# Optimization experiments

Measured on AMD Instinct MI355X. Metric: run time of the kernel, lower is better.

The kernel has to match this reference:

```python
import jax, jax.numpy as jnp
import numpy as np

EPS = 1e-5          # InstanceNorm eps (torch default)
KERNEL = 25         # moving_avg_kernel_size
TAU = 1.0           # gumbel softmax temperature
REGIME_NUM = 8


def _inorm(x):
    # InstanceNorm1d without affine on (N, C, L): normalize over last dim (biased var)
    m = x.mean(-1, keepdims=True)
    v = ((x - m) ** 2).mean(-1, keepdims=True)
    return (x - m) * jax.lax.rsqrt(v + EPS)


def _lbr(x, W, b):
    # Linear -> InstanceNorm (over last dim) -> exact GELU
    return jax.nn.gelu(_inorm(x @ W + b), approximate=False)


def _moving_avg(x, k):
    # x: (B, L, C); edge-replicate pad (k-1)//2 on both sides, sliding mean via cumsum
    p = (k - 1) // 2
    xp = jnp.concatenate([jnp.repeat(x[:, :1], p, axis=1), x,
                          jnp.repeat(x[:, -1:], p, axis=1)], axis=1)
    cs = jnp.concatenate([jnp.zeros_like(xp[:, :1]), jnp.cumsum(xp, axis=1)], axis=1)
    return (cs[:, k:] - cs[:, :-k]) / k  # (B, L, C)


def _encode(x, Ws, bs, Wt, bt):
    # inputs - inputs[:, 0:1]; series decomposition; seasonal+trend branches
    x = x - x[:, :1]
    mm = _moving_avg(x, KERNEL)
    return _lbr(x - mm, Ws, bs) + _lbr(mm, Wt, bt)  # (B, L, H)


def reference(inputs_longterm, inputs_shortterm,
              Ws, bs, Wt, bt,
              Wh1, bh1, Wl1, bl1, Wh2, bh2, Wl2, bl2, Wh3, bh3, Wl3, bl3,
              Wr, br, proto):
    e_lt = _encode(inputs_longterm, Ws, bs, Wt, bt)   # (B, L_lt, H)
    e_st = _encode(inputs_shortterm, Ws, bs, Wt, bt)  # (B, L_st, H)

    # RegimeEncoder: alternate hidden-dim and lookback-dim LinearBatchRelu layers
    o = _lbr(e_lt, Wh1, bh1)
    o = jnp.swapaxes(_lbr(jnp.swapaxes(o, 1, 2), Wl1, bl1), 1, 2)
    o = _lbr(o, Wh2, bh2)
    o = jnp.swapaxes(_lbr(jnp.swapaxes(o, 1, 2), Wl2, bl2), 1, 2)
    o = _lbr(o, Wh3, bh3)
    o = jnp.swapaxes(_lbr(jnp.swapaxes(o, 1, 2), Wl3, bl3), 1, 2)  # (B, L_lt//8, H)
    logits = o.reshape(o.shape[0], -1) @ Wr + br  # (B, R)

    # gumbel_softmax(hard=True) with straight-through estimator
    g = jax.random.gumbel(jax.random.key(42), logits.shape, logits.dtype)
    y_soft = jax.nn.softmax((logits + g) / TAU, axis=-1)
    y_hard = jax.nn.one_hot(jnp.argmax(y_soft, axis=-1), REGIME_NUM, dtype=logits.dtype)
    w = y_hard - jax.lax.stop_gradient(y_soft) + y_soft  # (B, R)

    # weighted sum over regime prototypes, then combine with encoded shortterm
    sel = jnp.einsum('br,rnhmo->bnhmo', w, proto)          # (B, L_st, H, M, 3)
    out = jnp.einsum('bnh,bnhmo->bmo', e_st, sel)          # (B, M, 3)
    B = out.shape[0]
    return jax.nn.softmax(out.reshape(B, -1), axis=-1).reshape(out.shape)


def setup_inputs() -> dict:
    key = jax.random.key(0)
    ks = jax.random.split(key, 24)
    B, L_lt, L_st, C, H, R, M = 32, 512, 128, 9, 128, 8, 64
    s = 0.02
    d = {
        'inputs_longterm':  jax.random.normal(ks[0], (B, L_lt, C), jnp.float32),
        'inputs_shortterm': jax.random.normal(ks[1], (B, L_st, C), jnp.float32),
        'Ws': jax.random.normal(ks[2], (C, H), jnp.float32) * s,
        'bs': jnp.zeros((H,), jnp.float32),
        'Wt': jax.random.normal(ks[3], (C, H), jnp.float32) * s,
        'bt': jnp.zeros((H,), jnp.float32),
        'Wh1': jax.random.normal(ks[4], (H, H), jnp.float32) * s,
        'bh1': jnp.zeros((H,), jnp.float32),
        'Wl1': jax.random.normal(ks[5], (L_lt, L_lt // 2), jnp.float32) * s,
        'bl1': jnp.zeros((L_lt // 2,), jnp.float32),
        'Wh2': jax.random.normal(ks[6], (H, H), jnp.float32) * s,
        'bh2': jnp.zeros((H,), jnp.float32),
        'Wl2': jax.random.normal(ks[7], (L_lt // 2, L_lt // 4), jnp.float32) * s,
        'bl2': jnp.zeros((L_lt // 4,), jnp.float32),
        'Wh3': jax.random.normal(ks[8], (H, H), jnp.float32) * s,
        'bh3': jnp.zeros((H,), jnp.float32),
        'Wl3': jax.random.normal(ks[9], (L_lt // 4, L_lt // 8), jnp.float32) * s,
        'bl3': jnp.zeros((L_lt // 8,), jnp.float32),
        'Wr': jax.random.normal(ks[10], (H * L_lt // 8, R), jnp.float32) * s,
        'br': jnp.zeros((R,), jnp.float32),
        'proto': jax.random.normal(ks[11], (R, L_st, H, M, 3), jnp.float32),
    }
    return d
```

## Files before the change

kernel.cpp:

```cpp
#include <hip/hip_runtime.h>
#include <math.h>

#define EPS 1e-5f

__device__ __forceinline__ float gelu_exact(float x) {
    return 0.5f * x * (1.0f + erff(x * 0.7071067811865476f));
}

__device__ float block_sum(float v, float* red) {
    int lane = threadIdx.x & 63, wid = threadIdx.x >> 6;
#pragma unroll
    for (int off = 32; off > 0; off >>= 1) v += __shfl_down(v, off, 64);
    if (lane == 0) red[wid] = v;
    __syncthreads();
    int nw = ((int)blockDim.x + 63) >> 6;
    float s = red[0];
    for (int w = 1; w < nw; w++) s += red[w];
    __syncthreads();
    return s;
}

__device__ float block_max(float v, float* red) {
    int lane = threadIdx.x & 63, wid = threadIdx.x >> 6;
#pragma unroll
    for (int off = 32; off > 0; off >>= 1) v = fmaxf(v, __shfl_down(v, off, 64));
    if (lane == 0) red[wid] = v;
    __syncthreads();
    int nw = ((int)blockDim.x + 63) >> 6;
    float s = red[0];
    for (int w = 1; w < nw; w++) s = fmaxf(s, red[w]);
    __syncthreads();
    return s;
}

__device__ void threefry2x32(unsigned k0, unsigned k1, unsigned x0, unsigned x1,
                             unsigned& o0, unsigned& o1) {
    unsigned ks[3] = {k0, k1, k0 ^ k1 ^ 0x1BD11BDAu};
    const unsigned rot[2][4] = {{13u, 15u, 26u, 6u}, {17u, 29u, 16u, 24u}};
    x0 += ks[0]; x1 += ks[1];
#pragma unroll
    for (int i = 0; i < 5; i++) {
#pragma unroll
        for (int j = 0; j < 4; j++) {
            unsigned r = rot[i & 1][j];
            x0 += x1;
            x1 = (x1 << r) | (x1 >> (32 - r));
            x1 ^= x0;
        }
        x0 += ks[(i + 1) % 3];
        x1 += ks[(i + 2) % 3] + (unsigned)(i + 1);
    }
    o0 = x0; o1 = x1;
}

__device__ float gumbel_at(int j) {
    unsigned o0, o1;
    threefry2x32(0u, 42u, 0u, (unsigned)j, o0, o1);
    unsigned bits = o0 ^ o1;
    float f = __uint_as_float((bits >> 9) | 0x3F800000u) - 1.0f;
    float u = fmaxf(f + 1.17549435e-38f, 1.17549435e-38f);
    return -logf(-logf(u));
}

__global__ __launch_bounds__(256) void encode_kernel(
    const float* __restrict__ x_lt, const float* __restrict__ x_st,
    const float* __restrict__ Ws, const float* __restrict__ bs,
    const float* __restrict__ Wt, const float* __restrict__ bt,
    float* __restrict__ e_lt, float* __restrict__ e_st) {
    const int b = blockIdx.y;
    const int w = threadIdx.x >> 6, ln = threadIdx.x & 63;
    const float* x; float* e; int L, l;
    if (blockIdx.x < 128) { x = x_lt; e = e_lt; L = 512; l = blockIdx.x * 4 + w; }
    else { x = x_st; e = e_st; L = 128; l = (blockIdx.x - 128) * 4 + w; }
    __shared__ float xw_all[4][228];
    __shared__ float sm_all[4][20];
    float* xw = xw_all[w];
    float* sm = sm_all[w];
    const float* xb = x + (size_t)b * L * 9;
#pragma unroll
    for (int q = 0; q < 4; q++) {
        int f = ln + 64 * q;
        if (f < 225) {
            int row = f / 9, c = f - row * 9;
            int rr = l - 12 + row;
            rr = rr < 0 ? 0 : (rr >= L ? L - 1 : rr);
            xw[f] = xb[(size_t)rr * 9 + c];
        }
    }
    __syncthreads();
    if (ln < 9) {
        float s = 0.f;
#pragma unroll
        for (int j = 0; j < 25; j++) s += xw[j * 9 + ln];
        float x0 = xb[ln];
        float mm = (s - 25.f * x0) * (1.0f / 25.0f);
        sm[ln] = (xw[108 + ln] - x0) - mm;
        sm[ln + 10] = mm;
    }
    __syncthreads();
    float ysA = bs[ln], ysB = bs[ln + 64];
    float ytA = bt[ln], ytB = bt[ln + 64];
#pragma unroll
    for (int c = 0; c < 9; c++) {
        float sv = sm[c], mv = sm[c + 10];
        ysA += sv * Ws[c * 128 + ln];
        ysB += sv * Ws[c * 128 + ln + 64];
        ytA += mv * Wt[c * 128 + ln];
        ytB += mv * Wt[c * 128 + ln + 64];
    }
    float sa = ysA + ysB, sb2 = ytA + ytB;
#pragma unroll
    for (int off = 32; off > 0; off >>= 1) {
        sa += __shfl_xor(sa, off, 64);
        sb2 += __shfl_xor(sb2, off, 64);
    }
    float ms = sa * (1.0f / 128.0f), mt = sb2 * (1.0f / 128.0f);
    float dA = ysA - ms, dB = ysB - ms;
    float tA = ytA - mt, tB = ytB - mt;
    float qa = dA * dA + dB * dB, qb = tA * tA + tB * tB;
#pragma unroll
    for (int off = 32; off > 0; off >>= 1) {
        qa += __shfl_xor(qa, off, 64);
        qb += __shfl_xor(qb, off, 64);
    }
    float inva = rsqrtf(qa * (1.0f / 128.0f) + EPS);
    float invb = rsqrtf(qb * (1.0f / 128.0f) + EPS);
    float* eo = e + ((size_t)b * L + l) * 128;
    eo[ln] = gelu_exact(dA * inva) + gelu_exact(tA * invb);
    eo[ln + 64] = gelu_exact(dB * inva) + gelu_exact(tB * invb);
}

template <int K, int N, int WR, bool TRANS>
__global__ __launch_bounds__(256) void lbr_wave(
    const float* __restrict__ A, int S, int ABOFF,
    const float* __restrict__ W, const float* __restrict__ bias,
    float* __restrict__ out, int OROWS, int OBOFF) {
    constexpr int CG = N / 4;
    constexpr int SG = 64 / CG;
    constexpr int RW = SG * WR;
    constexpr int MT = 4 * RW;
    constexpr int LOG2MT = (MT == 8) ? 3 : ((MT == 16) ? 4 : 5);
    constexpr int STAGE = 4 * RW * K;
    constexpr int TILE = TRANS ? MT * (N + 4) : 0;
    constexpr int LSZ = STAGE > TILE ? STAGE : TILE;
    __shared__ __align__(16) float lds[LSZ];
    const int t = threadIdx.x;
    const int w = t >> 6, ln = t & 63;
    const int sg = ln / CG;
    const int n0 = (ln % CG) * 4;
    const int b = blockIdx.y;
    const int r0b = blockIdx.x * MT;
    const int r0w = r0b + w * RW;
    float* As = lds + w * RW * K;
    const float* Ab = A + (size_t)b * ABOFF;
    for (int idx = ln; idx < RW * (K / 4); idx += 64) {
        int rr = idx / (K / 4), kk = idx % (K / 4);
        float4 v = *(const float4*)(Ab + (size_t)(r0w + rr) * S + kk * 4);
        *(float4*)(As + rr * K + kk * 4) = v;
    }
    float4 acc[WR];
    {
        float4 bv = *(const float4*)(bias + n0);
#pragma unroll
        for (int j = 0; j < WR; j++) acc[j] = bv;
    }
    const float* ap = As + (sg * WR) * K;
    const float* wp = W + n0;
#pragma unroll 2
    for (int k = 0; k < K; k += 4) {
        float4 w0 = *(const float4*)(wp);
        float4 w1 = *(const float4*)(wp + N);
        float4 w2 = *(const float4*)(wp + 2 * N);
        float4 w3 = *(const float4*)(wp + 3 * N);
        wp += 4 * N;
#pragma unroll
        for (int j = 0; j < WR; j++) {
            float4 a4 = *(const float4*)(ap + j * K + k);
            acc[j].x += a4.x * w0.x; acc[j].y += a4.x * w0.y;
            acc[j].z += a4.x * w0.z; acc[j].w += a4.x * w0.w;
            acc[j].x += a4.y * w1.x; acc[j].y += a4.y * w1.y;
            acc[j].z += a4.y * w1.z; acc[j].w += a4.y * w1.w;
            acc[j].x += a4.z * w2.x; acc[j].y += a4.z * w2.y;
            acc[j].z += a4.z * w2.z; acc[j].w += a4.z * w2.w;
            acc[j].x += a4.w * w3.x; acc[j].y += a4.w * w3.y;
            acc[j].z += a4.w * w3.z; acc[j].w += a4.w * w3.w;
        }
    }
    float4 res[WR];
#pragma unroll
    for (int j = 0; j < WR; j++) {
        float s = acc[j].x + acc[j].y + acc[j].z + acc[j].w;
#pragma unroll
        for (int off = CG / 2; off > 0; off >>= 1) s += __shfl_xor(s, off, 64);
        float m = s * (1.0f / (float)N);
        float dx = acc[j].x - m, dy = acc[j].y - m, dz = acc[j].z - m, dw = acc[j].w - m;
        float q = dx * dx + dy * dy + dz * dz + dw * dw;
#pragma unroll
        for (int off = CG / 2; off > 0; off >>= 1) q += __shfl_xor(q, off, 64);
        float inv = rsqrtf(q * (1.0f / (float)N) + EPS);
        res[j].x = gelu_exact(dx * inv);
        res[j].y = gelu_exact(dy * inv);
        res[j].z = gelu_exact(dz * inv);
        res[j].w = gelu_exact(dw * inv);
    }
    if constexpr (TRANS) {
        __syncthreads();
#pragma unroll
        for (int j = 0; j < WR; j++) {
            int rl = w * RW + sg * WR + j;
            *(float4*)(lds + rl * (N + 4) + n0) = res[j];
        }
        __syncthreads();
        float* ob = out + (size_t)b * OBOFF + r0b;
        for (int e = t; e < MT * N; e += 256) {
            int r = e & (MT - 1), n = e >> LOG2MT;
            ob[(size_t)n * OROWS + r] = lds[r * (N + 4) + n];
        }
    } else {
        float* ob = out + (size_t)b * OBOFF;
#pragma unroll
        for (int j = 0; j < WR; j++) {
            int row = r0w + sg * WR + j;
            *(float4*)(ob + (size_t)row * N + n0) = res[j];
        }
    }
}

__global__ __launch_bounds__(256) void logits_select(
    const float* __restrict__ O6, const float* __restrict__ Wr,
    const float* __restrict__ br, float* __restrict__ sel_w, int* __restrict__ sel_r) {
    int b = blockIdx.x, t = threadIdx.x;
    __shared__ float sO6[128 * 68];
    __shared__ float red[4][8];
    const float4* ob4 = (const float4*)(O6 + (size_t)b * 8192);
    for (int i4 = t; i4 < 2048; i4 += 256) {
        float4 v = ob4[i4];
        int p = i4 * 4;
        int h = p >> 6, l4 = p & 63;
        *(float4*)(&sO6[h * 68 + l4]) = v;
    }
    __syncthreads();
    float acc[8] = {0, 0, 0, 0, 0, 0, 0, 0};
#pragma unroll 4
    for (int q = 0; q < 32; q++) {
        int i = q * 256 + t;
        int l4 = i >> 7, h = i & 127;
        float v = sO6[h * 68 + l4];
        const float4* wr = (const float4*)(Wr + (size_t)i * 8);
        float4 w0 = wr[0], w1 = wr[1];
        acc[0] += v * w0.x; acc[1] += v * w0.y; acc[2] += v * w0.z; acc[3] += v * w0.w;
        acc[4] += v * w1.x; acc[5] += v * w1.y; acc[6] += v * w1.z; acc[7] += v * w1.w;
    }
#pragma unroll
    for (int j = 0; j < 8; j++)
#pragma unroll
        for (int off = 32; off > 0; off >>= 1) acc[j] += __shfl_xor(acc[j], off, 64);
    int lane = t & 63, wid = t >> 6;
    if (lane == 0)
        for (int j = 0; j < 8; j++) red[wid][j] = acc[j];
    __syncthreads();
    if (t == 0) {
        float z[8];
        for (int j = 0; j < 8; j++) {
            float lg = br[j] + red[0][j] + red[1][j] + red[2][j] + red[3][j];
            z[j] = lg + gumbel_at(b * 8 + j);
        }
        int am = 0;
        float zm = z[0];
        for (int j = 1; j < 8; j++)
            if (z[j] > zm) { zm = z[j]; am = j; }
        float ssum = 0.f;
        for (int j = 0; j < 8; j++) ssum += expf(z[j] - zm);
        float s = 1.0f / ssum;
        sel_w[b] = (1.0f - s) + s;
        sel_r[b] = am;
    }
}

__global__ __launch_bounds__(192, 4) void einsum_nsplit(
    const float* __restrict__ e_st, const float* __restrict__ proto,
    const int* __restrict__ sel_r, float* __restrict__ part) {
    const int n = blockIdx.x, r = blockIdx.y, hz = blockIdx.z, t = threadIdx.x;
    const int w = t >> 6, ln = t & 63;
    const int rg = ln >> 4;
    const int q4 = (w * 16 + (ln & 15)) * 4;
    __shared__ int loc[32];
    __shared__ int s_gs;
    if (t == 0) {
        int g = 0;
        for (int bb = 0; bb < 32; bb++)
            if (sel_r[bb] == r) loc[g++] = bb;
        s_gs = g;
    }
    __syncthreads();
    const int gs = s_gs;
    if (gs == 0) return;
    __shared__ __align__(16) float es[64][12];
    const float* pb = proto + (((size_t)r * 128 + n) * 128 + hz * 64) * 192;
    float* po = part + (size_t)hz * (32 * 128 * 192);
    for (int s0 = 0; s0 < gs; s0 += 8) {
        int np = gs - s0 < 8 ? gs - s0 : 8;
        __syncthreads();
        for (int i = t; i < 512; i += 192) {
            int sb = i >> 6, h = i & 63;
            float v = 0.f;
            if (sb < np)
                v = e_st[((size_t)loc[s0 + sb] * 128 + n) * 128 + hz * 64 + h];
            es[h][sb] = v;
        }
        __syncthreads();
        float4 a[8];
#pragma unroll
        for (int sb = 0; sb < 8; sb++) a[sb] = make_float4(0.f, 0.f, 0.f, 0.f);
#pragma unroll 4
        for (int hh = 0; hh < 16; hh++) {
            int row = hh * 4 + rg;
            float4 pv = *(const float4*)(pb + (size_t)row * 192 + q4);
            float4 e0 = *(const float4*)(&es[row][0]);
            float4 e1 = *(const float4*)(&es[row][4]);
#define ACC4(j, s) a[j].x += (s) * pv.x; a[j].y += (s) * pv.y; \
                   a[j].z += (s) * pv.z; a[j].w += (s) * pv.w;
            ACC4(0, e0.x) ACC4(1, e0.y) ACC4(2, e0.z) ACC4(3, e0.w)
            ACC4(4, e1.x) ACC4(5, e1.y) ACC4(6, e1.z) ACC4(7, e1.w)
#undef ACC4
        }
#pragma unroll
        for (int sb = 0; sb < 8; sb++) {
            a[sb].x += __shfl_xor(a[sb].x, 16, 64);
            a[sb].y += __shfl_xor(a[sb].y, 16, 64);
            a[sb].z += __shfl_xor(a[sb].z, 16, 64);
            a[sb].w += __shfl_xor(a[sb].w, 16, 64);
            a[sb].x += __shfl_xor(a[sb].x, 32, 64);
            a[sb].y += __shfl_xor(a[sb].y, 32, 64);
            a[sb].z += __shfl_xor(a[sb].z, 32, 64);
            a[sb].w += __shfl_xor(a[sb].w, 32, 64);
        }
        if (ln < 16) {
#pragma unroll
            for (int sb = 0; sb < 8; sb++) {
                if (sb < np) {
                    int bb = loc[s0 + sb];
                    *(float4*)(po + ((size_t)bb * 128 + n) * 192 + q4) = a[sb];
                }
            }
        }
    }
}

__global__ void finalize_kernel(const float* __restrict__ part, const float* __restrict__ sel_w,
                                float* __restrict__ out) {
    int b = blockIdx.x, t = threadIdx.x;
    __shared__ float red[4];
    const float* p0 = part + (size_t)b * 128 * 192 + t;
    const float* p1 = p0 + (size_t)32 * 128 * 192;
    float v = 0.f;
#pragma unroll 8
    for (int c = 0; c < 128; c++) {
        v += p0[(size_t)c * 192];
        v += p1[(size_t)c * 192];
    }
    v *= sel_w[b];
    float mx = block_max(v, red);
    float e = expf(v - mx);
    float s = block_sum(e, red);
    out[(size_t)b * 192 + t] = e / s;
}

extern "C" void kernel_launch(void* const* d_in, const int* in_sizes, int n_in,
                              void* d_out, int out_size, void* d_ws, size_t ws_size,
                              hipStream_t stream) {
    const float* in_lt = (const float*)d_in[0];
    const float* in_st = (const float*)d_in[1];
    const float* Ws  = (const float*)d_in[2];  const float* bs  = (const float*)d_in[3];
    const float* Wt  = (const float*)d_in[4];  const float* bt  = (const float*)d_in[5];
    const float* Wh1 = (const float*)d_in[6];  const float* bh1 = (const float*)d_in[7];
    const float* Wl1 = (const float*)d_in[8];  const float* bl1 = (const float*)d_in[9];
    const float* Wh2 = (const float*)d_in[10]; const float* bh2 = (const float*)d_in[11];
    const float* Wl2 = (const float*)d_in[12]; const float* bl2 = (const float*)d_in[13];
    const float* Wh3 = (const float*)d_in[14]; const float* bh3 = (const float*)d_in[15];
    const float* Wl3 = (const float*)d_in[16]; const float* bl3 = (const float*)d_in[17];
    const float* Wr  = (const float*)d_in[18]; const float* br  = (const float*)d_in[19];
    const float* proto = (const float*)d_in[20];
    float* out = (float*)d_out;

    float* ws = (float*)d_ws;
    size_t off = 0;
    float* e_lt = ws + off; off += (size_t)32 * 512 * 128;
    float* e_st = ws + off; off += (size_t)32 * 128 * 128;
    float* O1T = ws + off; off += (size_t)128 * 16384;
    float* O2T = ws + off; off += (size_t)256 * 4096;
    float* O3T = ws + off; off += (size_t)128 * 8192;
    float* O4T = ws + off; off += (size_t)128 * 4096;
    float* O5T = ws + off; off += (size_t)128 * 4096;
    float* O6 = ws + off; off += (size_t)32 * 128 * 64;
    float* part = ws + off; off += (size_t)2 * 32 * 128 * 192;
    float* sel_w = ws + off; off += 32;
    int* sel_r = (int*)(ws + off); off += 32;

    encode_kernel<<<dim3(160, 32), 256, 0, stream>>>(in_lt, in_st, Ws, bs, Wt, bt, e_lt, e_st);
    lbr_wave<128, 128, 4, true><<<dim3(512, 1), 256, 0, stream>>>(
        e_lt, 128, 0, Wh1, bh1, O1T, 16384, 0);
    lbr_wave<512, 256, 2, true><<<dim3(16, 32), 256, 0, stream>>>(
        O1T, 16384, 512, Wl1, bl1, O2T, 4096, 128);
    lbr_wave<128, 128, 2, true><<<dim3(16, 32), 256, 0, stream>>>(
        O2T, 4096, 128, Wh2, bh2, O3T, 8192, 256);
    lbr_wave<256, 128, 1, true><<<dim3(16, 32), 256, 0, stream>>>(
        O3T, 8192, 256, Wl2, bl2, O4T, 4096, 128);
    lbr_wave<128, 128, 1, true><<<dim3(16, 32), 256, 0, stream>>>(
        O4T, 4096, 128, Wh3, bh3, O5T, 4096, 128);
    lbr_wave<128, 64, 1, false><<<dim3(8, 32), 256, 0, stream>>>(
        O5T, 4096, 128, Wl3, bl3, O6, 0, 8192);
    logits_select<<<32, 256, 0, stream>>>(O6, Wr, br, sel_w, sel_r);
    einsum_nsplit<<<dim3(128, 8, 2), 192, 0, stream>>>(e_st, proto, sel_r, part);
    finalize_kernel<<<32, 192, 0, stream>>>(part, sel_w, out);
}
```

Measured before the change: 359.1 us.

## Stage weight chunks in LDS for lbr_wave GEMMs and shrink first-layer row tile

The per-thread global float4 loads of W in the LBR GEMM kernel are replaced by cooperative loads of K-chunks of W into shared memory, read back from LDS inside the inner loop. The A staging buffer now sits in its own region, and the TRANS output tile reuses the W region. The first layer halves rows per wave and doubles the grid. This cuts redundant global/L2 weight traffic across waves, at the cost of extra barriers per chunk and a larger LDS footprint that may lower occupancy.

```diff
diff --git a/kernel.cpp b/kernel.cpp
--- a/kernel.cpp
+++ b/kernel.cpp
@@ -130,7 +130,7 @@
     eo[ln + 64] = gelu_exact(dB * inva) + gelu_exact(tB * invb);
 }
 
-template <int K, int N, int WR, bool TRANS>
+template <int K, int N, int WR, int KC, bool TRANS>
 __global__ __launch_bounds__(256) void lbr_wave(
     const float* __restrict__ A, int S, int ABOFF,
     const float* __restrict__ W, const float* __restrict__ bias,
@@ -140,10 +140,11 @@
     constexpr int RW = SG * WR;
     constexpr int MT = 4 * RW;
     constexpr int LOG2MT = (MT == 8) ? 3 : ((MT == 16) ? 4 : 5);
-    constexpr int STAGE = 4 * RW * K;
-    constexpr int TILE = TRANS ? MT * (N + 4) : 0;
-    constexpr int LSZ = STAGE > TILE ? STAGE : TILE;
-    __shared__ __align__(16) float lds[LSZ];
+    constexpr int WSZ = KC * N;
+    constexpr int ASZ = 4 * RW * K;
+    static_assert(WSZ >= MT * (N + 4), "TRANS tile must fit in W region");
+    static_assert((WSZ / 4) % 256 == 0, "W chunk loads must be exact");
+    __shared__ __align__(16) float lds[WSZ + ASZ];
     const int t = threadIdx.x;
     const int w = t >> 6, ln = t & 63;
     const int sg = ln / CG;
@@ -151,7 +152,8 @@
     const int b = blockIdx.y;
     const int r0b = blockIdx.x * MT;
     const int r0w = r0b + w * RW;
-    float* As = lds + w * RW * K;
+    float* Wl = lds;
+    float* As = lds + WSZ + w * RW * K;
     const float* Ab = A + (size_t)b * ABOFF;
     for (int idx = ln; idx < RW * (K / 4); idx += 64) {
         int rr = idx / (K / 4), kk = idx % (K / 4);
@@ -165,25 +167,35 @@
         for (int j = 0; j < WR; j++) acc[j] = bv;
     }
     const float* ap = As + (sg * WR) * K;
-    const float* wp = W + n0;
+    for (int kc0 = 0; kc0 < K; kc0 += KC) {
+        __syncthreads();
+        {
+            const float4* wg = (const float4*)(W + (size_t)kc0 * N);
+            float4* wl4 = (float4*)Wl;
+#pragma unroll
+            for (int i = 0; i < WSZ / 4 / 256; i++)
+                wl4[t + i * 256] = wg[t + i * 256];
+        }
+        __syncthreads();
 #pragma unroll 2
-    for (int k = 0; k < K; k += 4) {
-        float4 w0 = *(const float4*)(wp);
-        float4 w1 = *(const float4*)(wp + N);
-        float4 w2 = *(const float4*)(wp + 2 * N);
-        float4 w3 = *(const float4*)(wp + 3 * N);
-        wp += 4 * N;
-#pragma unroll
-        for (int j = 0; j < WR; j++) {
-            float4 a4 = *(const float4*)(ap + j * K + k);
-            acc[j].x += a4.x * w0.x; acc[j].y += a4.x * w0.y;
-            acc[j].z += a4.x * w0.z; acc[j].w += a4.x * w0.w;
-            acc[j].x += a4.y * w1.x; acc[j].y += a4.y * w1.y;
-            acc[j].z += a4.y * w1.z; acc[j].w += a4.y * w1.w;
-            acc[j].x += a4.z * w2.x; acc[j].y += a4.z * w2.y;
-            acc[j].z += a4.z * w2.z; acc[j].w += a4.z * w2.w;
-            acc[j].x += a4.w * w3.x; acc[j].y += a4.w * w3.y;
-            acc[j].z += a4.w * w3.z; acc[j].w += a4.w * w3.w;
+        for (int k = 0; k < KC; k += 4) {
+            const float* wp = Wl + k * N + n0;
+            float4 w0 = *(const float4*)(wp);
+            float4 w1 = *(const float4*)(wp + N);
+            float4 w2 = *(const float4*)(wp + 2 * N);
+            float4 w3 = *(const float4*)(wp + 3 * N);
+#pragma unroll
+            for (int j = 0; j < WR; j++) {
+                float4 a4 = *(const float4*)(ap + j * K + kc0 + k);
+                acc[j].x += a4.x * w0.x; acc[j].y += a4.x * w0.y;
+                acc[j].z += a4.x * w0.z; acc[j].w += a4.x * w0.w;
+                acc[j].x += a4.y * w1.x; acc[j].y += a4.y * w1.y;
+                acc[j].z += a4.y * w1.z; acc[j].w += a4.y * w1.w;
+                acc[j].x += a4.z * w2.x; acc[j].y += a4.z * w2.y;
+                acc[j].z += a4.z * w2.z; acc[j].w += a4.z * w2.w;
+                acc[j].x += a4.w * w3.x; acc[j].y += a4.w * w3.y;
+                acc[j].z += a4.w * w3.z; acc[j].w += a4.w * w3.w;
+            }
         }
     }
     float4 res[WR];
@@ -398,17 +410,17 @@
     int* sel_r = (int*)(ws + off); off += 32;
 
     encode_kernel<<<dim3(160, 32), 256, 0, stream>>>(in_lt, in_st, Ws, bs, Wt, bt, e_lt, e_st);
-    lbr_wave<128, 128, 4, true><<<dim3(512, 1), 256, 0, stream>>>(
+    lbr_wave<128, 128, 2, 64, true><<<dim3(1024, 1), 256, 0, stream>>>(
         e_lt, 128, 0, Wh1, bh1, O1T, 16384, 0);
-    lbr_wave<512, 256, 2, true><<<dim3(16, 32), 256, 0, stream>>>(
+    lbr_wave<512, 256, 2, 32, true><<<dim3(16, 32), 256, 0, stream>>>(
         O1T, 16384, 512, Wl1, bl1, O2T, 4096, 128);
-    lbr_wave<128, 128, 2, true><<<dim3(16, 32), 256, 0, stream>>>(
+    lbr_wave<128, 128, 2, 64, true><<<dim3(16, 32), 256, 0, stream>>>(
         O2T, 4096, 128, Wh2, bh2, O3T, 8192, 256);
-    lbr_wave<256, 128, 1, true><<<dim3(16, 32), 256, 0, stream>>>(
+    lbr_wave<256, 128, 1, 64, true><<<dim3(16, 32), 256, 0, stream>>>(
         O3T, 8192, 256, Wl2, bl2, O4T, 4096, 128);
-    lbr_wave<128, 128, 1, true><<<dim3(16, 32), 256, 0, stream>>>(
+    lbr_wave<128, 128, 1, 64, true><<<dim3(16, 32), 256, 0, stream>>>(
         O4T, 4096, 128, Wh3, bh3, O5T, 4096, 128);
-    lbr_wave<128, 64, 1, false><<<dim3(8, 32), 256, 0, stream>>>(
+    lbr_wave<128, 64, 1, 128, false><<<dim3(8, 32), 256, 0, stream>>>(
         O5T, 4096, 128, Wl3, bl3, O6, 0, 8192);
     logits_select<<<32, 256, 0, stream>>>(O6, Wr, br, sel_w, sel_r);
     einsum_nsplit<<<dim3(128, 8, 2), 192, 0, stream>>>(e_st, proto, sel_r, part);
```

Result: faster. 321.8 us (-10.4%).
